# Kernel optimization log

Hardware: AMD Instinct MI355X
Metric: run time of the kernel (lower is better)

## Reference

```python
import jax, jax.numpy as jnp
from jax import lax
import numpy as np

B, S, E, H2, V = 128, 256, 256, 256, 50000  # batch, subword seq len, emb dim, per-direction hidden, vocab


def _make_masks(rng):
    # random subword lengths, word-start (bmask) and word-end (fmask) masks with equal counts per row
    lengths = rng.integers(S // 2, S + 1, size=B)
    pos = np.arange(S)[None, :]
    valid = pos < lengths[:, None]
    starts = (rng.random((B, S)) < 0.33) & valid
    starts[:, 0] = True
    nxt = np.concatenate([starts[:, 1:], np.zeros((B, 1), bool)], axis=1)
    fmask = valid & (nxt | (pos == lengths[:, None] - 1))
    return valid, fmask, starts


def setup_inputs():
    rng = np.random.default_rng(0)
    valid, fmask, bmask = _make_masks(rng)
    sw_ids = rng.integers(1, V, size=(B, S)) * valid  # 0 = pad
    key = jax.random.key(0)
    ks = jax.random.split(key, 8)
    se = float(np.sqrt(3.0 / E))       # random_embedding scale
    sh = float(1.0 / np.sqrt(H2))      # pytorch LSTM init scale
    u = lambda k, shape, s: jax.random.uniform(k, shape, jnp.float32, -s, s)
    return {
        "sw_ids": jnp.asarray(sw_ids, jnp.int32),
        "fmasks": jnp.asarray(fmask, jnp.int32),
        "bmasks": jnp.asarray(bmask, jnp.int32),
        "emb_W": u(ks[0], (V, E), se),
        "W_ih_f": u(ks[1], (4 * H2, E), sh),
        "W_hh_f": u(ks[2], (4 * H2, H2), sh),
        "b_f": u(ks[3], (4 * H2,), sh),
        "W_ih_b": u(ks[4], (4 * H2, E), sh),
        "W_hh_b": u(ks[5], (4 * H2, H2), sh),
        "b_b": u(ks[6], (4 * H2,), sh),
    }


def _lstm(x, mask, Wih, Whh, b):
    # x: [B,S,E]; mask: [B,S] float. Matches packed LSTM: state frozen and output
    # zeroed at padded steps (pad_packed_sequence zero-pads). Gate order i,f,g,o.
    h0 = jnp.zeros((x.shape[0], Whh.shape[1]), x.dtype)

    def step(carry, inp):
        h, c = carry
        xt, mt = inp
        g = xt @ Wih.T + h @ Whh.T + b
        i, f, gg, o = jnp.split(g, 4, axis=-1)
        c_new = jax.nn.sigmoid(f) * c + jax.nn.sigmoid(i) * jnp.tanh(gg)
        h_new = jax.nn.sigmoid(o) * jnp.tanh(c_new)
        m = mt[:, None]
        h = jnp.where(m > 0, h_new, h)
        c = jnp.where(m > 0, c_new, c)
        return (h, c), h * m

    _, ys = lax.scan(step, (h0, h0), (x.transpose(1, 0, 2), mask.T))
    return ys.transpose(1, 0, 2)  # [B,S,H2]


def _select_pad(out, mask, out_len):
    # vectorized masked_select + pad_sequence: stable-sort moves mask==1 positions
    # (in original order) to the front of the time axis, then zero beyond out_len.
    gather = jnp.argsort(1 - mask, axis=1)  # stable -> selected positions first
    sel = jnp.take_along_axis(out, gather[:, :, None], axis=1)
    word_valid = jnp.arange(out.shape[1])[None, :] < out_len[:, None]
    return sel * word_valid[:, :, None].astype(out.dtype)


def reference(sw_ids, fmasks, bmasks, emb_W, W_ih_f, W_hh_f, b_f, W_ih_b, W_hh_b, b_b):
    lengths = (sw_ids != 0).sum(axis=1)
    perm = jnp.argsort(-lengths)  # stable descending, like torch sort(descending=True)
    ids = sw_ids[perm]
    fm = fmasks[perm]
    bm = bmasks[perm]
    valid = (ids != 0).astype(emb_W.dtype)
    embeds = emb_W[ids]  # dropout is identity at eval time
    f_out = _lstm(embeds, valid, W_ih_f, W_hh_f, b_f)
    # backward direction: reverse in time (padding leads but state stays zero under mask)
    b_out = _lstm(embeds[:, ::-1], valid[:, ::-1], W_ih_b, W_hh_b, b_b)[:, ::-1]
    out_len = fm.sum(axis=1)
    f_pad = _select_pad(f_out, fm, out_len)
    b_pad = _select_pad(b_out, bm, out_len)
    perm2 = jnp.argsort(-out_len)
    out = jnp.concatenate([f_pad[perm2], b_pad[perm2]], axis=2)  # [B, S, 2*H2]
    return out, out_len[perm2]
```

## Files before the change

kernel.cpp:

```cpp
#include <hip/hip_runtime.h>
#include <hip/hip_bf16.h>
#include <hip/hip_fp16.h>
#include <math.h>
#include <stdint.h>

#define BB 128
#define SS 256
#define EE 256
#define HH 256
#define G4 1024
#define OUT_HEAD (BB*SS*2*HH)
#define SE 0.10825317547305482f

#define P8_HH_F 0
#define P8_HH_B 65536
#define P8_IH_F 131072
#define P8_IH_B 196608
#define SC_OFF  (1024*1024)
#define INT_OFF (1280*1024)
#define GX_OFF  (4*1024*1024)

typedef _Float16 h8v __attribute__((ext_vector_type(8)));

__device__ __forceinline__ float sigf(float x){ return 1.0f/(1.0f+__expf(-x)); }
__device__ __forceinline__ float tanhx(float x){
    float t = __expf(2.0f*x);
    return 1.0f - 2.0f/(t+1.0f);
}
__device__ __forceinline__ int dot4(uint32_t a, uint32_t b, int acc){
    return __builtin_amdgcn_sdot4((int)a, (int)b, acc, false);
}

__global__ __launch_bounds__(64) void pack8(const float* __restrict__ W,
    uint32_t* __restrict__ P8, float* __restrict__ SC){
    const int g = blockIdx.x, lane = threadIdx.x;
    float4 w4 = ((const float4*)(W + (size_t)g*EE))[lane];
    float m = fmaxf(fmaxf(fabsf(w4.x), fabsf(w4.y)), fmaxf(fabsf(w4.z), fabsf(w4.w)));
    for(int off=32; off; off>>=1) m = fmaxf(m, __shfl_xor(m, off));
    const float inv = (m > 0.f) ? 127.f/m : 0.f;
    int b0 = (int)rintf(w4.x*inv), b1 = (int)rintf(w4.y*inv);
    int b2 = (int)rintf(w4.z*inv), b3 = (int)rintf(w4.w*inv);
    uint32_t p = (uint32_t)(b0 & 0xff) | ((uint32_t)(b1 & 0xff) << 8) |
                 ((uint32_t)(b2 & 0xff) << 16) | ((uint32_t)(b3 & 0xff) << 24);
    P8[lane*G4 + g] = p;
    if(lane == 0) SC[g] = m / 127.f;
}

__global__ void prep(const int* __restrict__ sw, const int* __restrict__ fm,
                     const int* __restrict__ bm, int* __restrict__ wsI,
                     float* __restrict__ out_tail){
    __shared__ int len_s[BB], flen_s[BB], perm_s[BB], olp_s[BB];
    int b = threadIdx.x;
    int cnt = 0, fcnt = 0;
    for(int t=0;t<SS;t++){
        cnt  += (sw[b*SS+t] != 0);
        fcnt += fm[b*SS+t];
    }
    len_s[b] = cnt; flen_s[b] = fcnt;
    __syncthreads();
    int r = 0;
    for(int b2=0;b2<BB;b2++){
        int l2 = len_s[b2];
        r += (l2 > cnt) || (l2 == cnt && b2 < b);
    }
    perm_s[r] = b;
    __syncthreads();
    int orig = perm_s[b];
    olp_s[b] = flen_s[orig];
    wsI[0*BB + b] = orig;
    wsI[1*BB + b] = len_s[orig];
    __syncthreads();
    int v = olp_s[b];
    int q = 0;
    for(int r2=0;r2<BB;r2++){
        int v2 = olp_s[r2];
        q += (v2 > v) || (v2 == v && r2 < b);
    }
    wsI[2*BB + b] = q;
    wsI[3*BB + b] = v;
    out_tail[q] = (float)v;
    int* fdst = wsI + 4*BB;
    int* bdst = fdst + BB*SS;
    int fc = 0, bc = 0;
    for(int t=0;t<SS;t++){
        int fv = fm[orig*SS+t];
        fdst[b*SS+t] = (fv && fc < v) ? (q*SS + fc) : -1;
        fc += fv;
        int bv = bm[orig*SS+t];
        bdst[b*SS+t] = (bv && bc < v) ? (q*SS + bc) : -1;
        bc += bv;
    }
}

__global__ __launch_bounds__(1024)
__attribute__((amdgpu_waves_per_eu(4,4)))
void xg8g(const int* __restrict__ sw, const float* __restrict__ emb,
    const float* __restrict__ b_f, const float* __restrict__ b_b,
    const uint32_t* __restrict__ wsU, const float* __restrict__ scl,
    const int* __restrict__ wsI, _Float16* __restrict__ gx){
    __shared__ __align__(16) uint32_t xqT[64*64];
    const int tid = threadIdx.x, r = blockIdx.x, dir = blockIdx.y;
    const uint32_t* P = wsU + (dir ? P8_IH_B : P8_IH_F);
    const int gt = tid & 127;
    const int tt = tid >> 7;
    const int orig = wsI[r], L = wsI[BB + r];
    const int* ids = sw + orig*SS;
    _Float16* gxr = gx + ((size_t)(dir*BB + r))*SS*G4;
    const float* bias = dir ? b_b : b_f;
    const float* scA = scl + (2+dir)*G4;
    float bs[8], cs[8];
    #pragma unroll
    for(int k=0;k<8;k++){ bs[k] = bias[gt*8+k]; cs[k] = scA[gt*8+k]*(SE/127.f); }
    const int qtok = tid & 63, qg = tid >> 6;

    for(int t0 = 0; t0 < L; t0 += 64){
        int tq = t0 + qtok;
        #pragma unroll
        for(int q=0;q<4;q++){
            int d = qg + q*16;
            uint32_t pv = 0u;
            if(tq < L){
                float4 xf = ((const float4*)(emb + (size_t)ids[tq]*EE))[d];
                int b0=(int)rintf(xf.x*(127.f/SE)), b1=(int)rintf(xf.y*(127.f/SE));
                int b2=(int)rintf(xf.z*(127.f/SE)), b3=(int)rintf(xf.w*(127.f/SE));
                pv = (uint32_t)(b0 & 0xff) | ((uint32_t)(b1 & 0xff) << 8) |
                     ((uint32_t)(b2 & 0xff) << 16) | ((uint32_t)(b3 & 0xff) << 24);
            }
            xqT[d*64 + qtok] = pv;
        }
        __syncthreads();

        int acc[8][8];
        #pragma unroll
        for(int g=0;g<8;g++)
            #pragma unroll
            for(int k=0;k<8;k++) acc[g][k] = 0;

        #pragma unroll 2
        for(int j=0;j<64;j++){
            uint32_t wv[8], xv[8];
            *(uint4*)&wv[0] = *(const uint4*)&P[j*G4 + gt*8];
            *(uint4*)&wv[4] = *(const uint4*)&P[j*G4 + gt*8 + 4];
            *(uint4*)&xv[0] = *(const uint4*)&xqT[j*64 + tt*8];
            *(uint4*)&xv[4] = *(const uint4*)&xqT[j*64 + tt*8 + 4];
            #pragma unroll
            for(int g=0;g<8;g++)
                #pragma unroll
                for(int k=0;k<8;k++)
                    acc[g][k] = dot4(wv[g], xv[k], acc[g][k]);
        }

        #pragma unroll
        for(int k=0;k<8;k++){
            int t = t0 + tt*8 + k;
            if(t < L){
                h8v hv;
                #pragma unroll
                for(int g=0;g<8;g++) hv[g] = (_Float16)(bs[g] + (float)acc[g][k]*cs[g]);
                *((h8v*)(gxr + (size_t)t*G4 + gt*8)) = hv;
            }
        }
        __syncthreads();
    }
}

__global__ __launch_bounds__(1024)
__attribute__((amdgpu_waves_per_eu(4,4)))
void rec8L(const uint32_t* __restrict__ wsU, const float* __restrict__ scl,
    const int* __restrict__ wsI, const _Float16* __restrict__ gx,
    float* __restrict__ out){
    __shared__ __align__(16) uint32_t WC[32*1024];
    __shared__ float gfl[G4];
    __shared__ int h8i[64];
    const int tid = threadIdx.x, r = blockIdx.x, dir = blockIdx.y;
    const uint32_t* P = wsU + (dir ? P8_HH_B : P8_HH_F);
    #pragma unroll
    for(int j=0;j<32;j++){
        uint32_t v = P[j*G4 + tid];
        WC[tid*32 + (((j>>2) ^ (tid&7))<<2) + (j&3)] = v;
    }
    const float csh = scl[dir*G4 + tid] * (1.f/127.f);
    const int L = wsI[BB + r];
    const int* dstA = wsI + 4*BB + (dir ? BB*SS : 0) + r*SS;
    if(tid < 64) h8i[tid] = 0;
    float cst = 0.f;
    const _Float16* gxr = gx + ((size_t)(dir*BB + r))*SS*G4;
    const int t0 = dir ? L-1 : 0, stp = dir ? -1 : 1;
    _Float16 gv = gxr[(size_t)t0*G4 + tid];
    __syncthreads();

    for(int s=0;s<L;s++){
        const int t = t0 + s*stp;
        const float gxv = (float)gv;
        if(s+1 < L) gv = gxr[(size_t)(t+stp)*G4 + tid];
        uint32_t ws[32];
        #pragma unroll
        for(int m=0;m<32;m++) ws[m] = P[(32+m)*G4 + tid];
        uint32_t wc[32];
        #pragma unroll
        for(int jg=0;jg<8;jg++)
            *(uint4*)&wc[jg*4] = *(const uint4*)&WC[tid*32 + ((jg ^ (tid&7))<<2)];
        int acc0 = 0, acc1 = 0;
        const uint4* hp = (const uint4*)h8i;
        #pragma unroll
        for(int q=0;q<8;q++){
            uint4 hv = hp[q];
            acc0 = dot4(wc[q*4+0], hv.x, acc0);
            acc1 = dot4(wc[q*4+1], hv.y, acc1);
            acc0 = dot4(wc[q*4+2], hv.z, acc0);
            acc1 = dot4(wc[q*4+3], hv.w, acc1);
        }
        #pragma unroll
        for(int q=0;q<8;q++){
            uint4 hv = hp[8+q];
            acc0 = dot4(ws[q*4+0], hv.x, acc0);
            acc1 = dot4(ws[q*4+1], hv.y, acc1);
            acc0 = dot4(ws[q*4+2], hv.z, acc0);
            acc1 = dot4(ws[q*4+3], hv.w, acc1);
        }
        gfl[tid] = gxv + (float)(acc0 + acc1)*csh;
        __syncthreads();
        if(tid < HH){
            float gi = gfl[tid], gf = gfl[tid+256], gz = gfl[tid+512], go = gfl[tid+768];
            float i = sigf(gi), f = sigf(gf), z = tanhx(gz), o = sigf(go);
            cst = f*cst + i*z;
            float hn = o*tanhx(cst);
            ((signed char*)h8i)[tid] = (signed char)(int)rintf(hn*127.f);
            int dst = dstA[t];
            if(dst >= 0) out[(size_t)dst*(2*HH) + dir*HH + tid] = hn;
        }
        __syncthreads();
    }
}

extern "C" void kernel_launch(void* const* d_in, const int* in_sizes, int n_in,
                              void* d_out, int out_size, void* d_ws, size_t ws_size,
                              hipStream_t stream){
    const int*   sw    = (const int*)d_in[0];
    const int*   fm    = (const int*)d_in[1];
    const int*   bm    = (const int*)d_in[2];
    const float* emb   = (const float*)d_in[3];
    const float* Wih_f = (const float*)d_in[4];
    const float* Whh_f = (const float*)d_in[5];
    const float* b_f   = (const float*)d_in[6];
    const float* Wih_b = (const float*)d_in[7];
    const float* Whh_b = (const float*)d_in[8];
    const float* b_b   = (const float*)d_in[9];
    float* out = (float*)d_out;
    uint32_t* wsU = (uint32_t*)d_ws;
    float* scl = (float*)((char*)d_ws + SC_OFF);
    int* wsI = (int*)((char*)d_ws + INT_OFF);
    _Float16* gxp = (_Float16*)((char*)d_ws + GX_OFF);

    hipMemsetAsync(d_out, 0, (size_t)out_size*4, stream);
    pack8<<<G4, 64, 0, stream>>>(Whh_f, wsU + P8_HH_F, scl + 0*G4);
    pack8<<<G4, 64, 0, stream>>>(Whh_b, wsU + P8_HH_B, scl + 1*G4);
    pack8<<<G4, 64, 0, stream>>>(Wih_f, wsU + P8_IH_F, scl + 2*G4);
    pack8<<<G4, 64, 0, stream>>>(Wih_b, wsU + P8_IH_B, scl + 3*G4);
    prep<<<1, BB, 0, stream>>>(sw, fm, bm, wsI, out + OUT_HEAD);
    xg8g<<<dim3(BB,2), 1024, 0, stream>>>(sw, emb, b_f, b_b, wsU, scl, wsI, gxp);
    rec8L<<<dim3(BB,2), 1024, 0, stream>>>(wsU, scl, wsI, gxp, out);
}
```

Before: 596.6 us.

## Quantize recurrent weights to 4-bit and retile input-gate GEMM

Recurrent weight matrices are packed as offset-binary 4-bit nibbles. The recurrence kernel reads them directly from global memory instead of splitting between LDS and global, and corrects the offset with a per-step sum of the quantized hidden state computed by a wave reduction. The input-gate kernel is retiled to 32-token chunks with 4 gates per thread. This halves recurrent weight traffic and frees LDS, but adds a reduction to the serial step and loses accuracy from 4-bit weights.

```diff
diff --git a/kernel.cpp b/kernel.cpp
--- a/kernel.cpp
+++ b/kernel.cpp
@@ -11,16 +11,17 @@
 #define G4 1024
 #define OUT_HEAD (BB*SS*2*HH)
 #define SE 0.10825317547305482f
-
-#define P8_HH_F 0
-#define P8_HH_B 65536
+#define QX (127.0f/SE)
+
+#define P4_HH_F 0
+#define P4_HH_B 32768
 #define P8_IH_F 131072
 #define P8_IH_B 196608
 #define SC_OFF  (1024*1024)
 #define INT_OFF (1280*1024)
 #define GX_OFF  (4*1024*1024)
 
-typedef _Float16 h8v __attribute__((ext_vector_type(8)));
+typedef _Float16 h4v __attribute__((ext_vector_type(4)));
 
 __device__ __forceinline__ float sigf(float x){ return 1.0f/(1.0f+__expf(-x)); }
 __device__ __forceinline__ float tanhx(float x){
@@ -46,6 +47,22 @@
     if(lane == 0) SC[g] = m / 127.f;
 }
 
+__global__ __launch_bounds__(64) void pack4(const float* __restrict__ W,
+    uint32_t* __restrict__ P4, float* __restrict__ SC){
+    const int g = blockIdx.x, lane = threadIdx.x;
+    float4 w4 = ((const float4*)(W + (size_t)g*EE))[lane];
+    float m = fmaxf(fmaxf(fabsf(w4.x), fabsf(w4.y)), fmaxf(fabsf(w4.z), fabsf(w4.w)));
+    for(int off=32; off; off>>=1) m = fmaxf(m, __shfl_xor(m, off));
+    const float inv = (m > 0.f) ? 7.f/m : 0.f;
+    int q0 = (int)rintf(w4.x*inv) + 8, q1 = (int)rintf(w4.y*inv) + 8;
+    int q2 = (int)rintf(w4.z*inv) + 8, q3 = (int)rintf(w4.w*inv) + 8;
+    uint32_t mypack = (uint32_t)q0 | ((uint32_t)q1 << 8) |
+                      ((uint32_t)q2 << 16) | ((uint32_t)q3 << 24);
+    uint32_t other = __shfl_xor(mypack, 1);
+    if(!(lane & 1)) P4[(size_t)g*32 + (lane>>1)] = mypack | (other << 4);
+    if(lane == 0) SC[g] = m / 7.f;
+}
+
 __global__ void prep(const int* __restrict__ sw, const int* __restrict__ fm,
                      const int* __restrict__ bm, int* __restrict__ wsI,
                      float* __restrict__ out_tail){
@@ -94,70 +111,76 @@
 
 __global__ __launch_bounds__(1024)
 __attribute__((amdgpu_waves_per_eu(4,4)))
-void xg8g(const int* __restrict__ sw, const float* __restrict__ emb,
+void xg32(const int* __restrict__ sw, const float* __restrict__ emb,
     const float* __restrict__ b_f, const float* __restrict__ b_b,
     const uint32_t* __restrict__ wsU, const float* __restrict__ scl,
     const int* __restrict__ wsI, _Float16* __restrict__ gx){
-    __shared__ __align__(16) uint32_t xqT[64*64];
+    __shared__ __align__(16) uint32_t xqT[64*32];
     const int tid = threadIdx.x, r = blockIdx.x, dir = blockIdx.y;
     const uint32_t* P = wsU + (dir ? P8_IH_B : P8_IH_F);
-    const int gt = tid & 127;
-    const int tt = tid >> 7;
+    const int gt = tid & 255;
+    const int tt = tid >> 8;
     const int orig = wsI[r], L = wsI[BB + r];
     const int* ids = sw + orig*SS;
     _Float16* gxr = gx + ((size_t)(dir*BB + r))*SS*G4;
     const float* bias = dir ? b_b : b_f;
     const float* scA = scl + (2+dir)*G4;
-    float bs[8], cs[8];
+    float bs[4], cs[4];
     #pragma unroll
-    for(int k=0;k<8;k++){ bs[k] = bias[gt*8+k]; cs[k] = scA[gt*8+k]*(SE/127.f); }
-    const int qtok = tid & 63, qg = tid >> 6;
-
-    for(int t0 = 0; t0 < L; t0 += 64){
-        int tq = t0 + qtok;
-        #pragma unroll
-        for(int q=0;q<4;q++){
-            int d = qg + q*16;
+    for(int g=0;g<4;g++){ bs[g] = bias[gt*4+g]; cs[g] = scA[gt*4+g]*(SE/127.f); }
+    const int kq = tid & 31, dq = tid >> 5;
+
+    for(int t0 = 0; t0 < L; t0 += 32){
+        int tq = t0 + kq;
+        #pragma unroll
+        for(int q=0;q<2;q++){
+            int d = dq + q*32;
             uint32_t pv = 0u;
-            if(tq < L){
+            if(tq < L && d < 64){
                 float4 xf = ((const float4*)(emb + (size_t)ids[tq]*EE))[d];
-                int b0=(int)rintf(xf.x*(127.f/SE)), b1=(int)rintf(xf.y*(127.f/SE));
-                int b2=(int)rintf(xf.z*(127.f/SE)), b3=(int)rintf(xf.w*(127.f/SE));
+                int b0=(int)rintf(xf.x*QX), b1=(int)rintf(xf.y*QX);
+                int b2=(int)rintf(xf.z*QX), b3=(int)rintf(xf.w*QX);
                 pv = (uint32_t)(b0 & 0xff) | ((uint32_t)(b1 & 0xff) << 8) |
                      ((uint32_t)(b2 & 0xff) << 16) | ((uint32_t)(b3 & 0xff) << 24);
             }
-            xqT[d*64 + qtok] = pv;
-        }
-        __syncthreads();
-
-        int acc[8][8];
-        #pragma unroll
-        for(int g=0;g<8;g++)
+            if(d < 64) xqT[d*32 + kq] = pv;
+        }
+        __syncthreads();
+
+        int acc[4][8];
+        #pragma unroll
+        for(int g=0;g<4;g++)
             #pragma unroll
             for(int k=0;k<8;k++) acc[g][k] = 0;
 
-        #pragma unroll 2
+        const uint4* xv4 = (const uint4*)xqT;
+        #pragma unroll 4
         for(int j=0;j<64;j++){
-            uint32_t wv[8], xv[8];
-            *(uint4*)&wv[0] = *(const uint4*)&P[j*G4 + gt*8];
-            *(uint4*)&wv[4] = *(const uint4*)&P[j*G4 + gt*8 + 4];
-            *(uint4*)&xv[0] = *(const uint4*)&xqT[j*64 + tt*8];
-            *(uint4*)&xv[4] = *(const uint4*)&xqT[j*64 + tt*8 + 4];
+            uint4 wv = *(const uint4*)&P[j*G4 + gt*4];
+            uint4 xa = xv4[j*8 + tt*2];
+            uint4 xb = xv4[j*8 + tt*2 + 1];
             #pragma unroll
-            for(int g=0;g<8;g++)
-                #pragma unroll
-                for(int k=0;k<8;k++)
-                    acc[g][k] = dot4(wv[g], xv[k], acc[g][k]);
+            for(int g=0;g<4;g++){
+                uint32_t w = ((const uint32_t*)&wv)[g];
+                acc[g][0] = dot4(w, xa.x, acc[g][0]);
+                acc[g][1] = dot4(w, xa.y, acc[g][1]);
+                acc[g][2] = dot4(w, xa.z, acc[g][2]);
+                acc[g][3] = dot4(w, xa.w, acc[g][3]);
+                acc[g][4] = dot4(w, xb.x, acc[g][4]);
+                acc[g][5] = dot4(w, xb.y, acc[g][5]);
+                acc[g][6] = dot4(w, xb.z, acc[g][6]);
+                acc[g][7] = dot4(w, xb.w, acc[g][7]);
+            }
         }
 
         #pragma unroll
         for(int k=0;k<8;k++){
             int t = t0 + tt*8 + k;
             if(t < L){
-                h8v hv;
+                h4v hv;
                 #pragma unroll
-                for(int g=0;g<8;g++) hv[g] = (_Float16)(bs[g] + (float)acc[g][k]*cs[g]);
-                *((h8v*)(gxr + (size_t)t*G4 + gt*8)) = hv;
+                for(int g=0;g<4;g++) hv[g] = (_Float16)(bs[g] + (float)acc[g][k]*cs[g]);
+                *((h4v*)(gxr + (size_t)t*G4 + gt*4)) = hv;
             }
         }
         __syncthreads();
@@ -166,23 +189,19 @@
 
 __global__ __launch_bounds__(1024)
 __attribute__((amdgpu_waves_per_eu(4,4)))
-void rec8L(const uint32_t* __restrict__ wsU, const float* __restrict__ scl,
+void rec4(const uint32_t* __restrict__ wsU, const float* __restrict__ scl,
     const int* __restrict__ wsI, const _Float16* __restrict__ gx,
     float* __restrict__ out){
-    __shared__ __align__(16) uint32_t WC[32*1024];
     __shared__ float gfl[G4];
     __shared__ int h8i[64];
+    __shared__ int hsp[4];
     const int tid = threadIdx.x, r = blockIdx.x, dir = blockIdx.y;
-    const uint32_t* P = wsU + (dir ? P8_HH_B : P8_HH_F);
-    #pragma unroll
-    for(int j=0;j<32;j++){
-        uint32_t v = P[j*G4 + tid];
-        WC[tid*32 + (((j>>2) ^ (tid&7))<<2) + (j&3)] = v;
-    }
+    const uint32_t* P = wsU + (dir ? P4_HH_B : P4_HH_F) + (size_t)tid*32;
     const float csh = scl[dir*G4 + tid] * (1.f/127.f);
     const int L = wsI[BB + r];
     const int* dstA = wsI + 4*BB + (dir ? BB*SS : 0) + r*SS;
     if(tid < 64) h8i[tid] = 0;
+    if(tid < 4) hsp[tid] = 0;
     float cst = 0.f;
     const _Float16* gxr = gx + ((size_t)(dir*BB + r))*SS*G4;
     const int t0 = dir ? L-1 : 0, stp = dir ? -1 : 1;
@@ -193,39 +212,35 @@
         const int t = t0 + s*stp;
         const float gxv = (float)gv;
         if(s+1 < L) gv = gxr[(size_t)(t+stp)*G4 + tid];
-        uint32_t ws[32];
-        #pragma unroll
-        for(int m=0;m<32;m++) ws[m] = P[(32+m)*G4 + tid];
-        uint32_t wc[32];
-        #pragma unroll
-        for(int jg=0;jg<8;jg++)
-            *(uint4*)&wc[jg*4] = *(const uint4*)&WC[tid*32 + ((jg ^ (tid&7))<<2)];
+        const int sum_h = hsp[0] + hsp[1] + hsp[2] + hsp[3];
         int acc0 = 0, acc1 = 0;
-        const uint4* hp = (const uint4*)h8i;
-        #pragma unroll
-        for(int q=0;q<8;q++){
-            uint4 hv = hp[q];
-            acc0 = dot4(wc[q*4+0], hv.x, acc0);
-            acc1 = dot4(wc[q*4+1], hv.y, acc1);
-            acc0 = dot4(wc[q*4+2], hv.z, acc0);
-            acc1 = dot4(wc[q*4+3], hv.w, acc1);
-        }
-        #pragma unroll
-        for(int q=0;q<8;q++){
-            uint4 hv = hp[8+q];
-            acc0 = dot4(ws[q*4+0], hv.x, acc0);
-            acc1 = dot4(ws[q*4+1], hv.y, acc1);
-            acc0 = dot4(ws[q*4+2], hv.z, acc0);
-            acc1 = dot4(ws[q*4+3], hv.w, acc1);
-        }
-        gfl[tid] = gxv + (float)(acc0 + acc1)*csh;
+        const uint4* hp4 = (const uint4*)h8i;
+        #pragma unroll
+        for(int i=0;i<8;i++){
+            uint4 wp = ((const uint4*)P)[i];
+            uint4 h0 = hp4[2*i], h1 = hp4[2*i+1];
+            const uint32_t M = 0x0F0F0F0Fu;
+            acc0 = dot4( wp.x       & M, h0.x, acc0);
+            acc1 = dot4((wp.x >> 4) & M, h0.y, acc1);
+            acc0 = dot4( wp.y       & M, h0.z, acc0);
+            acc1 = dot4((wp.y >> 4) & M, h0.w, acc1);
+            acc0 = dot4( wp.z       & M, h1.x, acc0);
+            acc1 = dot4((wp.z >> 4) & M, h1.y, acc1);
+            acc0 = dot4( wp.w       & M, h1.z, acc0);
+            acc1 = dot4((wp.w >> 4) & M, h1.w, acc1);
+        }
+        gfl[tid] = gxv + (float)(acc0 + acc1 - 8*sum_h)*csh;
         __syncthreads();
         if(tid < HH){
             float gi = gfl[tid], gf = gfl[tid+256], gz = gfl[tid+512], go = gfl[tid+768];
             float i = sigf(gi), f = sigf(gf), z = tanhx(gz), o = sigf(go);
             cst = f*cst + i*z;
             float hn = o*tanhx(cst);
-            ((signed char*)h8i)[tid] = (signed char)(int)rintf(hn*127.f);
+            int hq = (int)rintf(hn*127.f);
+            ((signed char*)h8i)[tid] = (signed char)hq;
+            int sh = hq;
+            for(int off=32; off; off>>=1) sh += __shfl_xor(sh, off);
+            if((tid & 63) == 0) hsp[tid >> 6] = sh;
             int dst = dstA[t];
             if(dst >= 0) out[(size_t)dst*(2*HH) + dir*HH + tid] = hn;
         }
@@ -253,11 +268,11 @@
     _Float16* gxp = (_Float16*)((char*)d_ws + GX_OFF);
 
     hipMemsetAsync(d_out, 0, (size_t)out_size*4, stream);
-    pack8<<<G4, 64, 0, stream>>>(Whh_f, wsU + P8_HH_F, scl + 0*G4);
-    pack8<<<G4, 64, 0, stream>>>(Whh_b, wsU + P8_HH_B, scl + 1*G4);
+    pack4<<<G4, 64, 0, stream>>>(Whh_f, wsU + P4_HH_F, scl + 0*G4);
+    pack4<<<G4, 64, 0, stream>>>(Whh_b, wsU + P4_HH_B, scl + 1*G4);
     pack8<<<G4, 64, 0, stream>>>(Wih_f, wsU + P8_IH_F, scl + 2*G4);
     pack8<<<G4, 64, 0, stream>>>(Wih_b, wsU + P8_IH_B, scl + 3*G4);
     prep<<<1, BB, 0, stream>>>(sw, fm, bm, wsI, out + OUT_HEAD);
-    xg8g<<<dim3(BB,2), 1024, 0, stream>>>(sw, emb, b_f, b_b, wsU, scl, wsI, gxp);
-    rec8L<<<dim3(BB,2), 1024, 0, stream>>>(wsU, scl, wsI, gxp, out);
-}
+    xg32<<<dim3(BB,2), 1024, 0, stream>>>(sw, emb, b_f, b_b, wsU, scl, wsI, gxp);
+    rec4<<<dim3(BB,2), 1024, 0, stream>>>(wsU, scl, wsI, gxp, out);
+}
```

Result: faster. 566.8 us (-5.0%).
